# Kernel optimization log

Measured on AMD Instinct MI355X. Metric: run time of the kernel, lower is better.

The kernel has to match this reference:

```python
import jax, jax.numpy as jnp
import numpy as np

B, V, E, W = 1024, 50257, 128, 4  # batch, vocab, embed, CBOW window

def setup_inputs() -> dict:
    key = jax.random.key(0)
    k1, k2, k3, k4 = jax.random.split(key, 4)
    # near-one-hot averaged bag-of-words: 2*W context indices per row, each weighted 1/(2*W)
    ctx_idx = jax.random.randint(k1, (B, 2 * W), 0, V)
    xs = jnp.zeros((B, V), dtype=jnp.float32).at[jnp.arange(B)[:, None], ctx_idx].add(1.0 / (2 * W))
    metric = jax.random.normal(k2, (E, E), dtype=jnp.float32)  # unused by forward, kept for signature fidelity
    EMBEDM = jax.random.normal(k3, (V, E), dtype=jnp.float32)
    embed2vocab = jax.random.normal(k4, (E, V), dtype=jnp.float32)
    return {"xs": xs, "metric": metric, "EMBEDM": EMBEDM, "embed2vocab": embed2vocab}

def reference(xs, metric, EMBEDM, embed2vocab):
    # [B,V] @ [V,E] -> [B,E]  (gather+average in disguise: xs is sparse n-hot)
    xsembeds = xs @ EMBEDM
    # [B,E] @ [E,V] -> [B,V], then row-wise log_softmax
    xsouts = xsembeds @ embed2vocab
    return jax.nn.log_softmax(xsouts, axis=1)
```

## Files before the change

### kernel.cpp

```cpp
#include <hip/hip_runtime.h>
#include <hip/hip_bf16.h>

#define B_ROWS 1024
#define V_DIM 50257
#define E_DIM 128
#define V_PAD 50304

typedef __attribute__((ext_vector_type(8))) short short8;
typedef __attribute__((ext_vector_type(4))) float float4v;

__global__ void k0_transpose(const float* __restrict__ e2v,
                             __hip_bfloat16* __restrict__ e2vT) {
    __shared__ float t[32][33];
    const int v0 = blockIdx.x * 32;
    const int k0 = blockIdx.y * 32;
    const int c = threadIdx.x & 31;
    const int r = threadIdx.x >> 5;
#pragma unroll
    for (int i = 0; i < 4; ++i) {
        const int k = k0 + r + i * 8;
        const int v = v0 + c;
        t[r + i * 8][c] = (v < V_DIM) ? e2v[(size_t)k * V_DIM + v] : 0.0f;
    }
    __syncthreads();
#pragma unroll
    for (int i = 0; i < 4; ++i) {
        const int rv = r + i * 8;
        e2vT[(size_t)(v0 + rv) * E_DIM + k0 + c] = __float2bfloat16(t[c][rv]);
    }
}

__global__ void k1_embed(const float* __restrict__ xs,
                         const float* __restrict__ EM,
                         __hip_bfloat16* __restrict__ xse) {
    const int b = blockIdx.x;
    const int tid = threadIdx.x;
    __shared__ int nzv[64];
    __shared__ float nzval[64];
    __shared__ int nzcount;
    if (tid == 0) nzcount = 0;
    __syncthreads();

    const size_t base = (size_t)b * V_DIM;
    auto note = [&](int v, float val) {
        if (val != 0.0f) {
            int s = atomicAdd(&nzcount, 1);
            if (s < 64) { nzv[s] = v; nzval[s] = val; }
        }
    };

    const int h = (int)((4 - (base & 3)) & 3);
    if (tid < h) note(tid, xs[base + tid]);
    const int n4 = (V_DIM - h) >> 2;
    const float4* xv = reinterpret_cast<const float4*>(xs + base + h);
    for (int j = tid; j < n4; j += 256) {
        float4 x = xv[j];
        if (x.x != 0.0f || x.y != 0.0f || x.z != 0.0f || x.w != 0.0f) {
            const int v = h + 4 * j;
            note(v + 0, x.x);
            note(v + 1, x.y);
            note(v + 2, x.z);
            note(v + 3, x.w);
        }
    }
    for (int i = h + n4 * 4 + tid; i < V_DIM; i += 256) note(i, xs[base + i]);
    __syncthreads();

    int cnt = nzcount;
    if (cnt > 64) cnt = 64;
    if (tid < E_DIM) {
        float a = 0.0f;
        for (int s = 0; s < cnt; ++s)
            a += nzval[s] * EM[(size_t)nzv[s] * E_DIM + tid];
        xse[(size_t)b * E_DIM + tid] = __float2bfloat16(a);
    }
}

__global__ __launch_bounds__(256) void k2_gemm(
        const __hip_bfloat16* __restrict__ xse,
        const __hip_bfloat16* __restrict__ e2vT,
        float* __restrict__ out) {
    __shared__ unsigned short As[128][136];
    __shared__ unsigned short Bs[64][136];
    const int tid = threadIdx.x;
    const int m0 = blockIdx.x * 128;
    const int v0 = blockIdx.y * 64;

    const unsigned short* gA = reinterpret_cast<const unsigned short*>(xse);
    const unsigned short* gB = reinterpret_cast<const unsigned short*>(e2vT);

#pragma unroll
    for (int i = 0; i < 8; ++i) {
        const int c = tid + i * 256;
        const int row = c >> 4;
        const int kc = (c & 15) << 3;
        *reinterpret_cast<int4*>(&As[row][kc]) =
            *reinterpret_cast<const int4*>(gA + (size_t)(m0 + row) * E_DIM + kc);
    }
#pragma unroll
    for (int i = 0; i < 4; ++i) {
        const int c = tid + i * 256;
        const int row = c >> 4;
        const int kc = (c & 15) << 3;
        *reinterpret_cast<int4*>(&Bs[row][kc]) =
            *reinterpret_cast<const int4*>(gB + (size_t)(v0 + row) * E_DIM + kc);
    }
    __syncthreads();

    const int w = tid >> 6;
    const int lane = tid & 63;
    const int q = lane >> 4;
    const int l16 = lane & 15;
    const int wm = w * 32;

    float4v acc[2][4];
#pragma unroll
    for (int mi = 0; mi < 2; ++mi)
#pragma unroll
        for (int ni = 0; ni < 4; ++ni)
            acc[mi][ni] = (float4v){0.0f, 0.0f, 0.0f, 0.0f};

#pragma unroll
    for (int kk = 0; kk < 128; kk += 32) {
        const int ko = kk + q * 8;
        short8 a0 = *reinterpret_cast<const short8*>(&As[wm + l16][ko]);
        short8 a1 = *reinterpret_cast<const short8*>(&As[wm + 16 + l16][ko]);
#pragma unroll
        for (int ni = 0; ni < 4; ++ni) {
            short8 bf = *reinterpret_cast<const short8*>(&Bs[ni * 16 + l16][ko]);
            acc[0][ni] = __builtin_amdgcn_mfma_f32_16x16x32_bf16(a0, bf, acc[0][ni], 0, 0, 0);
            acc[1][ni] = __builtin_amdgcn_mfma_f32_16x16x32_bf16(a1, bf, acc[1][ni], 0, 0, 0);
        }
    }

#pragma unroll
    for (int ni = 0; ni < 4; ++ni) {
        const int col = v0 + ni * 16 + l16;
        if (col < V_DIM) {
#pragma unroll
            for (int mi = 0; mi < 2; ++mi) {
                const int rbase = m0 + wm + mi * 16 + q * 4;
#pragma unroll
                for (int r = 0; r < 4; ++r)
                    out[(size_t)(rbase + r) * V_DIM + col] = acc[mi][ni][r];
            }
        }
    }
}

__global__ void k3_lse(const float* __restrict__ logits,
                       float* __restrict__ stats) {
    const int b = blockIdx.x;
    const int tid = threadIdx.x;
    const size_t base = (size_t)b * V_DIM;

    float m = -INFINITY, s = 0.0f;
    auto upd = [&](float x) {
        if (x > m) { s = s * __expf(m - x) + 1.0f; m = x; }
        else       { s += __expf(x - m); }
    };

    const int h = (int)((4 - (base & 3)) & 3);
    if (tid < h) upd(logits[base + tid]);
    const int n4 = (V_DIM - h) >> 2;
    const float4* lv = reinterpret_cast<const float4*>(logits + base + h);
    for (int j = tid; j < n4; j += 256) {
        float4 x = lv[j];
        upd(x.x); upd(x.y); upd(x.z); upd(x.w);
    }
    for (int i = h + n4 * 4 + tid; i < V_DIM; i += 256) upd(logits[base + i]);

    __shared__ float rm[256], rs[256];
    rm[tid] = m; rs[tid] = s;
    __syncthreads();
    for (int off = 128; off > 0; off >>= 1) {
        if (tid < off) {
            const float m2 = rm[tid + off], s2 = rs[tid + off];
            const float M = fmaxf(m, m2);
            s = s * __expf(m - M) + s2 * __expf(m2 - M);
            m = M;
            rm[tid] = m; rs[tid] = s;
        }
        __syncthreads();
    }
    if (tid == 0) stats[b] = m + __logf(s);
}

__global__ void k4_norm(float* __restrict__ out,
                        const float* __restrict__ stats) {
    const unsigned total4 = (unsigned)((size_t)B_ROWS * V_DIM / 4);
    const unsigned stride = gridDim.x * blockDim.x;
    float4* o4 = reinterpret_cast<float4*>(out);
    for (unsigned i = blockIdx.x * blockDim.x + threadIdx.x; i < total4; i += stride) {
        float4 x = o4[i];
        const unsigned flat = i * 4u;
        const unsigned b0 = flat / V_DIM;
        const unsigned r = flat - b0 * V_DIM;
        if (r + 3 < V_DIM) {
            const float l = stats[b0];
            x.x -= l; x.y -= l; x.z -= l; x.w -= l;
        } else {
            x.x -= stats[(flat + 0) / V_DIM];
            x.y -= stats[(flat + 1) / V_DIM];
            x.z -= stats[(flat + 2) / V_DIM];
            x.w -= stats[(flat + 3) / V_DIM];
        }
        o4[i] = x;
    }
}

extern "C" void kernel_launch(void* const* d_in, const int* in_sizes, int n_in,
                              void* d_out, int out_size, void* d_ws, size_t ws_size,
                              hipStream_t stream) {
    const float* xs  = (const float*)d_in[0];
    const float* EM  = (const float*)d_in[2];
    const float* e2v = (const float*)d_in[3];
    float* out = (float*)d_out;

    char* ws = (char*)d_ws;
    __hip_bfloat16* e2vT = (__hip_bfloat16*)ws;
    __hip_bfloat16* xse  = (__hip_bfloat16*)(ws + (size_t)V_PAD * E_DIM * 2);
    float* stats = (float*)(ws + (size_t)V_PAD * E_DIM * 2 + (size_t)B_ROWS * E_DIM * 2);

    hipLaunchKernelGGL(k0_transpose, dim3(V_PAD / 32, E_DIM / 32), dim3(256), 0, stream, e2v, e2vT);
    hipLaunchKernelGGL(k1_embed, dim3(B_ROWS), dim3(256), 0, stream, xs, EM, xse);
    hipLaunchKernelGGL(k2_gemm, dim3(B_ROWS / 128, (V_DIM + 63) / 64), dim3(256), 0, stream, xse, e2vT, out);
    hipLaunchKernelGGL(k3_lse, dim3(B_ROWS), dim3(256), 0, stream, out, stats);
    hipLaunchKernelGGL(k4_norm, dim3(4096), dim3(256), 0, stream, out, stats);
}
```

Baseline: 500.6 us.

## Fuse log-softmax stats into GEMM and recompute GEMM for normalized write

Replaces the write-logits, read-for-LSE, read-modify-write normalize sequence with two GEMM passes. The first pass computes per-tile row max and sum-exp in registers and writes only small partials. A combine kernel reduces these partials to per-row log-sum-exp. A second GEMM pass recomputes the logits and writes the normalized output once. This removes about three full passes over the roughly 200 MB output at the cost of running the cheap K=128 GEMM twice.

```diff
diff --git a/kernel.cpp b/kernel.cpp
--- a/kernel.cpp
+++ b/kernel.cpp
@@ -5,6 +5,7 @@
 #define V_DIM 50257
 #define E_DIM 128
 #define V_PAD 50304
+#define NCT 786
 
 typedef __attribute__((ext_vector_type(8))) short short8;
 typedef __attribute__((ext_vector_type(4))) float float4v;
@@ -76,100 +77,109 @@
     }
 }
 
-__global__ __launch_bounds__(256) void k2_gemm(
+#define GEMM_TILE_BODY(xse, e2vT)                                              \
+    __shared__ unsigned short As[128][136];                                    \
+    __shared__ unsigned short Bs[64][136];                                     \
+    const int tid = threadIdx.x;                                               \
+    const int m0 = blockIdx.x * 128;                                           \
+    const int v0 = blockIdx.y * 64;                                            \
+    const unsigned short* gA = reinterpret_cast<const unsigned short*>(xse);   \
+    const unsigned short* gB = reinterpret_cast<const unsigned short*>(e2vT);  \
+    _Pragma("unroll")                                                          \
+    for (int i = 0; i < 8; ++i) {                                              \
+        const int c = tid + i * 256;                                           \
+        const int row = c >> 4;                                                \
+        const int kc = (c & 15) << 3;                                          \
+        *reinterpret_cast<int4*>(&As[row][kc]) =                               \
+            *reinterpret_cast<const int4*>(gA + (size_t)(m0 + row) * E_DIM + kc); \
+    }                                                                          \
+    _Pragma("unroll")                                                          \
+    for (int i = 0; i < 4; ++i) {                                              \
+        const int c = tid + i * 256;                                           \
+        const int row = c >> 4;                                                \
+        const int kc = (c & 15) << 3;                                          \
+        *reinterpret_cast<int4*>(&Bs[row][kc]) =                               \
+            *reinterpret_cast<const int4*>(gB + (size_t)(v0 + row) * E_DIM + kc); \
+    }                                                                          \
+    __syncthreads();                                                           \
+    const int w = tid >> 6;                                                    \
+    const int lane = tid & 63;                                                 \
+    const int q = lane >> 4;                                                   \
+    const int l16 = lane & 15;                                                 \
+    const int wm = w * 32;                                                     \
+    float4v acc[2][4];                                                         \
+    _Pragma("unroll")                                                          \
+    for (int mi = 0; mi < 2; ++mi)                                             \
+        _Pragma("unroll")                                                      \
+        for (int ni = 0; ni < 4; ++ni)                                         \
+            acc[mi][ni] = (float4v){0.0f, 0.0f, 0.0f, 0.0f};                   \
+    _Pragma("unroll")                                                          \
+    for (int kk = 0; kk < 128; kk += 32) {                                     \
+        const int ko = kk + q * 8;                                             \
+        short8 a0 = *reinterpret_cast<const short8*>(&As[wm + l16][ko]);       \
+        short8 a1 = *reinterpret_cast<const short8*>(&As[wm + 16 + l16][ko]);  \
+        _Pragma("unroll")                                                      \
+        for (int ni = 0; ni < 4; ++ni) {                                       \
+            short8 bf = *reinterpret_cast<const short8*>(&Bs[ni * 16 + l16][ko]); \
+            acc[0][ni] = __builtin_amdgcn_mfma_f32_16x16x32_bf16(a0, bf, acc[0][ni], 0, 0, 0); \
+            acc[1][ni] = __builtin_amdgcn_mfma_f32_16x16x32_bf16(a1, bf, acc[1][ni], 0, 0, 0); \
+        }                                                                      \
+    }
+
+__global__ __launch_bounds__(256) void kb_pass1(
         const __hip_bfloat16* __restrict__ xse,
         const __hip_bfloat16* __restrict__ e2vT,
-        float* __restrict__ out) {
-    __shared__ unsigned short As[128][136];
-    __shared__ unsigned short Bs[64][136];
-    const int tid = threadIdx.x;
-    const int m0 = blockIdx.x * 128;
-    const int v0 = blockIdx.y * 64;
-
-    const unsigned short* gA = reinterpret_cast<const unsigned short*>(xse);
-    const unsigned short* gB = reinterpret_cast<const unsigned short*>(e2vT);
-
-#pragma unroll
-    for (int i = 0; i < 8; ++i) {
-        const int c = tid + i * 256;
-        const int row = c >> 4;
-        const int kc = (c & 15) << 3;
-        *reinterpret_cast<int4*>(&As[row][kc]) =
-            *reinterpret_cast<const int4*>(gA + (size_t)(m0 + row) * E_DIM + kc);
-    }
-#pragma unroll
-    for (int i = 0; i < 4; ++i) {
-        const int c = tid + i * 256;
-        const int row = c >> 4;
-        const int kc = (c & 15) << 3;
-        *reinterpret_cast<int4*>(&Bs[row][kc]) =
-            *reinterpret_cast<const int4*>(gB + (size_t)(v0 + row) * E_DIM + kc);
-    }
-    __syncthreads();
-
-    const int w = tid >> 6;
-    const int lane = tid & 63;
-    const int q = lane >> 4;
-    const int l16 = lane & 15;
-    const int wm = w * 32;
-
-    float4v acc[2][4];
-#pragma unroll
-    for (int mi = 0; mi < 2; ++mi)
-#pragma unroll
-        for (int ni = 0; ni < 4; ++ni)
-            acc[mi][ni] = (float4v){0.0f, 0.0f, 0.0f, 0.0f};
-
-#pragma unroll
-    for (int kk = 0; kk < 128; kk += 32) {
-        const int ko = kk + q * 8;
-        short8 a0 = *reinterpret_cast<const short8*>(&As[wm + l16][ko]);
-        short8 a1 = *reinterpret_cast<const short8*>(&As[wm + 16 + l16][ko]);
-#pragma unroll
-        for (int ni = 0; ni < 4; ++ni) {
-            short8 bf = *reinterpret_cast<const short8*>(&Bs[ni * 16 + l16][ko]);
-            acc[0][ni] = __builtin_amdgcn_mfma_f32_16x16x32_bf16(a0, bf, acc[0][ni], 0, 0, 0);
-            acc[1][ni] = __builtin_amdgcn_mfma_f32_16x16x32_bf16(a1, bf, acc[1][ni], 0, 0, 0);
-        }
-    }
-
-#pragma unroll
-    for (int ni = 0; ni < 4; ++ni) {
-        const int col = v0 + ni * 16 + l16;
-        if (col < V_DIM) {
-#pragma unroll
-            for (int mi = 0; mi < 2; ++mi) {
-                const int rbase = m0 + wm + mi * 16 + q * 4;
-#pragma unroll
-                for (int r = 0; r < 4; ++r)
-                    out[(size_t)(rbase + r) * V_DIM + col] = acc[mi][ni][r];
-            }
-        }
-    }
-}
-
-__global__ void k3_lse(const float* __restrict__ logits,
-                       float* __restrict__ stats) {
+        float* __restrict__ pmax,
+        float* __restrict__ psum) {
+    GEMM_TILE_BODY(xse, e2vT)
+
+#pragma unroll
+    for (int mi = 0; mi < 2; ++mi) {
+#pragma unroll
+        for (int r = 0; r < 4; ++r) {
+            float mx = -INFINITY;
+#pragma unroll
+            for (int ni = 0; ni < 4; ++ni) {
+                const int col = v0 + ni * 16 + l16;
+                const float x = (col < V_DIM) ? acc[mi][ni][r] : -INFINITY;
+                mx = fmaxf(mx, x);
+            }
+            mx = fmaxf(mx, __shfl_xor(mx, 1));
+            mx = fmaxf(mx, __shfl_xor(mx, 2));
+            mx = fmaxf(mx, __shfl_xor(mx, 4));
+            mx = fmaxf(mx, __shfl_xor(mx, 8));
+            float s = 0.0f;
+#pragma unroll
+            for (int ni = 0; ni < 4; ++ni) {
+                const int col = v0 + ni * 16 + l16;
+                const float x = (col < V_DIM) ? acc[mi][ni][r] : -INFINITY;
+                s += __expf(x - mx);
+            }
+            s += __shfl_xor(s, 1);
+            s += __shfl_xor(s, 2);
+            s += __shfl_xor(s, 4);
+            s += __shfl_xor(s, 8);
+            if (l16 == 0) {
+                const int row = m0 + wm + mi * 16 + q * 4 + r;
+                pmax[(size_t)row * NCT + blockIdx.y] = mx;
+                psum[(size_t)row * NCT + blockIdx.y] = s;
+            }
+        }
+    }
+}
+
+__global__ void kc_combine(const float* __restrict__ pmax,
+                           const float* __restrict__ psum,
+                           float* __restrict__ stats) {
     const int b = blockIdx.x;
     const int tid = threadIdx.x;
-    const size_t base = (size_t)b * V_DIM;
-
     float m = -INFINITY, s = 0.0f;
-    auto upd = [&](float x) {
-        if (x > m) { s = s * __expf(m - x) + 1.0f; m = x; }
-        else       { s += __expf(x - m); }
-    };
-
-    const int h = (int)((4 - (base & 3)) & 3);
-    if (tid < h) upd(logits[base + tid]);
-    const int n4 = (V_DIM - h) >> 2;
-    const float4* lv = reinterpret_cast<const float4*>(logits + base + h);
-    for (int j = tid; j < n4; j += 256) {
-        float4 x = lv[j];
-        upd(x.x); upd(x.y); upd(x.z); upd(x.w);
-    }
-    for (int i = h + n4 * 4 + tid; i < V_DIM; i += 256) upd(logits[base + i]);
-
+    for (int j = tid; j < NCT; j += 256) {
+        const float mj = pmax[(size_t)b * NCT + j];
+        const float sj = psum[(size_t)b * NCT + j];
+        if (mj > m) { s = s * __expf(m - mj) + sj; m = mj; }
+        else        { s += sj * __expf(mj - m); }
+    }
     __shared__ float rm[256], rs[256];
     rm[tid] = m; rs[tid] = s;
     __syncthreads();
@@ -186,26 +196,28 @@
     if (tid == 0) stats[b] = m + __logf(s);
 }
 
-__global__ void k4_norm(float* __restrict__ out,
-                        const float* __restrict__ stats) {
-    const unsigned total4 = (unsigned)((size_t)B_ROWS * V_DIM / 4);
-    const unsigned stride = gridDim.x * blockDim.x;
-    float4* o4 = reinterpret_cast<float4*>(out);
-    for (unsigned i = blockIdx.x * blockDim.x + threadIdx.x; i < total4; i += stride) {
-        float4 x = o4[i];
-        const unsigned flat = i * 4u;
-        const unsigned b0 = flat / V_DIM;
-        const unsigned r = flat - b0 * V_DIM;
-        if (r + 3 < V_DIM) {
-            const float l = stats[b0];
-            x.x -= l; x.y -= l; x.z -= l; x.w -= l;
-        } else {
-            x.x -= stats[(flat + 0) / V_DIM];
-            x.y -= stats[(flat + 1) / V_DIM];
-            x.z -= stats[(flat + 2) / V_DIM];
-            x.w -= stats[(flat + 3) / V_DIM];
-        }
-        o4[i] = x;
+__global__ __launch_bounds__(256) void kd_pass2(
+        const __hip_bfloat16* __restrict__ xse,
+        const __hip_bfloat16* __restrict__ e2vT,
+        const float* __restrict__ stats,
+        float* __restrict__ out) {
+    GEMM_TILE_BODY(xse, e2vT)
+
+#pragma unroll
+    for (int mi = 0; mi < 2; ++mi) {
+        const int rbase = m0 + wm + mi * 16 + q * 4;
+        float l[4];
+#pragma unroll
+        for (int r = 0; r < 4; ++r) l[r] = stats[rbase + r];
+#pragma unroll
+        for (int ni = 0; ni < 4; ++ni) {
+            const int col = v0 + ni * 16 + l16;
+            if (col < V_DIM) {
+#pragma unroll
+                for (int r = 0; r < 4; ++r)
+                    out[(size_t)(rbase + r) * V_DIM + col] = acc[mi][ni][r] - l[r];
+            }
+        }
     }
 }
 
@@ -219,12 +231,18 @@
 
     char* ws = (char*)d_ws;
     __hip_bfloat16* e2vT = (__hip_bfloat16*)ws;
-    __hip_bfloat16* xse  = (__hip_bfloat16*)(ws + (size_t)V_PAD * E_DIM * 2);
-    float* stats = (float*)(ws + (size_t)V_PAD * E_DIM * 2 + (size_t)B_ROWS * E_DIM * 2);
+    size_t off = (size_t)V_PAD * E_DIM * 2;
+    __hip_bfloat16* xse = (__hip_bfloat16*)(ws + off);
+    off += (size_t)B_ROWS * E_DIM * 2;
+    float* pmax = (float*)(ws + off);
+    off += (size_t)B_ROWS * NCT * 4;
+    float* psum = (float*)(ws + off);
+    off += (size_t)B_ROWS * NCT * 4;
+    float* stats = (float*)(ws + off);
 
     hipLaunchKernelGGL(k0_transpose, dim3(V_PAD / 32, E_DIM / 32), dim3(256), 0, stream, e2v, e2vT);
     hipLaunchKernelGGL(k1_embed, dim3(B_ROWS), dim3(256), 0, stream, xs, EM, xse);
-    hipLaunchKernelGGL(k2_gemm, dim3(B_ROWS / 128, (V_DIM + 63) / 64), dim3(256), 0, stream, xse, e2vT, out);
-    hipLaunchKernelGGL(k3_lse, dim3(B_ROWS), dim3(256), 0, stream, out, stats);
-    hipLaunchKernelGGL(k4_norm, dim3(4096), dim3(256), 0, stream, out, stats);
-}
+    hipLaunchKernelGGL(kb_pass1, dim3(B_ROWS / 128, NCT), dim3(256), 0, stream, xse, e2vT, pmax, psum);
+    hipLaunchKernelGGL(kc_combine, dim3(B_ROWS), dim3(256), 0, stream, pmax, psum, stats);
+    hipLaunchKernelGGL(kd_pass2, dim3(B_ROWS / 128, NCT), dim3(256), 0, stream, xse, e2vT, stats, out);
+}
```

After: 460.4 us. 1.09x faster.
